# Kernel tuning notes

Hardware: AMD Instinct MI355X
Metric: run time of the kernel (lower is better)

Reference implementation:

```python
import jax, jax.numpy as jnp
import numpy as np

EPS = 1e-08
IN_CH = 256
OUT_CH = 256
STYLE_DIM = 256
B, N = 4, 65536


def setup_inputs() -> dict:
    key = jax.random.key(0)
    k1, k2, k3, k4 = jax.random.split(key, 4)
    x = jax.random.normal(k1, (B, N, IN_CH), dtype=jnp.float32)
    style = jax.random.normal(k2, (B, N, STYLE_DIM), dtype=jnp.float32)
    # base weight: torch.randn(1,1,in,out) * sqrt(2/(1+0.2^2)) / sqrt(in)
    w_scale = np.sqrt(2.0 / (1.0 + 0.2 ** 2)) / np.sqrt(IN_CH)
    weight = jax.random.normal(k3, (IN_CH, OUT_CH), dtype=jnp.float32) * w_scale
    bias = jnp.zeros((OUT_CH,), dtype=jnp.float32)
    # affine Linear(style_dim -> in_channel), kaiming normal fan_in linear: std = 1/sqrt(fan_in)
    affine_w = jax.random.normal(k4, (IN_CH, STYLE_DIM), dtype=jnp.float32) / np.sqrt(STYLE_DIM)
    affine_b = jnp.zeros((IN_CH,), dtype=jnp.float32)
    return {"x": x, "style": style, "weight": weight, "bias": bias,
            "affine_w": affine_w, "affine_b": affine_b}


def reference(x, style, weight, bias, affine_w, affine_b):
    # mod[b,n,i] = affine(style) + 1
    mod = jnp.einsum('bns,is->bni', style, affine_w) + affine_b + 1.0
    # out0[b,n,o] = sum_i x[b,n,i] * mod[b,n,i] * weight[i,o]
    out0 = jnp.einsum('bni,io->bno', x * mod, weight)
    # demod[b,n,o] = rsqrt(sum_i (weight[i,o]*mod[b,n,i])^2 + eps)
    ssq = jnp.einsum('bni,io->bno', mod * mod, weight * weight)  # [B,N,out]
    out = out0 * jax.lax.rsqrt(ssq + EPS)
    return out + bias
```

## Files before the change

### kernel.cpp

```cpp
#include <hip/hip_runtime.h>


#define CH   256
#define BM   64
#define EPS  1e-8f

typedef __attribute__((ext_vector_type(4))) float f32x4;
typedef __attribute__((ext_vector_type(8))) short bf16x8;
typedef __attribute__((ext_vector_type(4))) short s16x4;

__device__ __forceinline__ short f2b(float f) {
    __bf16 h = (__bf16)f;
    return __builtin_bit_cast(short, h);
}
__device__ __forceinline__ float b2f(short b) {
    union { unsigned u; float f; } v;
    v.u = ((unsigned)(unsigned short)b) << 16;
    return v.f;
}
__device__ __forceinline__ int swz(int row, int chunk) {
    return row * 512 + ((chunk ^ (row & 7)) << 4);
}

__global__ void prep_kernel(const float* __restrict__ weight,
                            const float* __restrict__ affw,
                            short* __restrict__ wTb, short* __restrict__ wT2b,
                            short* __restrict__ affwb)
{
    int t = threadIdx.x, b = blockIdx.x;
    float w  = weight[t * CH + b];
    short wb = f2b(w);
    float wf = b2f(wb);
    wTb  [b * CH + t] = wb;
    wT2b [b * CH + t] = f2b(wf * wf);
    affwb[b * CH + t] = f2b(affw[b * CH + t]);
}

__global__ __launch_bounds__(512, 4)
void smod_main(const float* __restrict__ x, const float* __restrict__ style,
               const float* __restrict__ bias, const float* __restrict__ affb,
               const short* __restrict__ wTb, const short* __restrict__ wT2b,
               const short* __restrict__ affwb,
               float* __restrict__ out)
{
    __shared__ __align__(16) unsigned char smem[65536];
    char* regA = (char*)smem;
    char* regB = (char*)smem + 32768;

    const int tid  = threadIdx.x;
    const int lane = tid & 63;
    const int wid  = tid >> 6;
    const int l15  = lane & 15;
    const int lgrp = lane >> 4;
    const int koff = lgrp << 3;
    const long r0  = (long)blockIdx.x * BM;

    const int urow = (wid << 1) + (lane >> 5);
    const int uch  = lane & 31;

    f32x4 sld[4][2];
    #pragma unroll
    for (int k = 0; k < 4; ++k) {
        const float* p = style + (r0 + k * 16 + urow) * CH + uch * 8;
        sld[k][0] = *(const f32x4*)p;
        sld[k][1] = *(const f32x4*)(p + 4);
    }
    f32x4 xld[4][2];
    #pragma unroll
    for (int k = 0; k < 4; ++k) {
        const float* p = x + (r0 + k * 16 + urow) * CH + uch * 8;
        xld[k][0] = *(const f32x4*)p;
        xld[k][1] = *(const f32x4*)(p + 4);
    }
    #pragma unroll
    for (int k = 0; k < 4; ++k) {
        int row = k * 16 + urow;
        bf16x8 v;
        #pragma unroll
        for (int j = 0; j < 8; ++j)
            v[j] = f2b(j < 4 ? sld[k][0][j] : sld[k][1][j - 4]);
        *(bf16x8*)(regA + swz(row, uch)) = v;
    }
    __syncthreads();

    f32x4 accm[2][4];
    #pragma unroll
    for (int a = 0; a < 2; ++a)
        #pragma unroll
        for (int b = 0; b < 4; ++b) { accm[a][b][0]=0.f; accm[a][b][1]=0.f; accm[a][b][2]=0.f; accm[a][b][3]=0.f; }

    #pragma unroll
    for (int kc = 0; kc < 8; ++kc) {
        bf16x8 af[2];
        #pragma unroll
        for (int it = 0; it < 2; ++it)
            af[it] = *(const bf16x8*)(affwb + (wid * 32 + it * 16 + l15) * CH + kc * 32 + koff);
        #pragma unroll
        for (int rt = 0; rt < 4; ++rt) {
            bf16x8 bfr = *(const bf16x8*)(regA + swz(rt * 16 + l15, kc * 4 + lgrp));
            #pragma unroll
            for (int it = 0; it < 2; ++it)
                accm[it][rt] = __builtin_amdgcn_mfma_f32_16x16x32_bf16(
                    af[it], bfr, accm[it][rt], 0, 0, 0);
        }
    }

    #pragma unroll
    for (int it = 0; it < 2; ++it) {
        int i0 = wid * 32 + it * 16 + (lgrp << 2);
        f32x4 ab = *(const f32x4*)(affb + i0);
        int chunk = i0 >> 3;
        int sub   = (i0 & 7) << 1;
        #pragma unroll
        for (int rt = 0; rt < 4; ++rt) {
            int row = rt * 16 + l15;
            f32x4 m = accm[it][rt];
            s16x4 o4 = { f2b(m[0] + ab[0] + 1.0f), f2b(m[1] + ab[1] + 1.0f),
                         f2b(m[2] + ab[2] + 1.0f), f2b(m[3] + ab[3] + 1.0f) };
            *(s16x4*)(regB + swz(row, chunk) + sub) = o4;
        }
    }
    __syncthreads();

    #pragma unroll
    for (int k = 0; k < 4; ++k) {
        int row = k * 16 + urow;
        bf16x8 mb = *(const bf16x8*)(regB + swz(row, uch));
        bf16x8 a1v, a2v;
        #pragma unroll
        for (int j = 0; j < 8; ++j) {
            float mf = b2f(mb[j]);
            float xf = (j < 4) ? xld[k][0][j] : xld[k][1][j - 4];
            a1v[j] = f2b(xf * mf);
            a2v[j] = f2b(mf * mf);
        }
        *(bf16x8*)(regA + swz(row, uch)) = a1v;
        *(bf16x8*)(regB + swz(row, uch)) = a2v;
    }
    __syncthreads();

    f32x4 acc0[4][2], acc1[4][2];
    #pragma unroll
    for (int a = 0; a < 4; ++a)
        #pragma unroll
        for (int b = 0; b < 2; ++b) {
            acc0[a][b][0]=0.f; acc0[a][b][1]=0.f; acc0[a][b][2]=0.f; acc0[a][b][3]=0.f;
            acc1[a][b][0]=0.f; acc1[a][b][1]=0.f; acc1[a][b][2]=0.f; acc1[a][b][3]=0.f;
        }

    #pragma unroll
    for (int kc = 0; kc < 8; ++kc) {
        bf16x8 bw[2], bw2[2];
        #pragma unroll
        for (int ct = 0; ct < 2; ++ct) {
            int o = wid * 32 + ct * 16 + l15;
            bw [ct] = *(const bf16x8*)(wTb  + o * CH + kc * 32 + koff);
            bw2[ct] = *(const bf16x8*)(wT2b + o * CH + kc * 32 + koff);
        }
        #pragma unroll
        for (int rt = 0; rt < 4; ++rt) {
            int row = rt * 16 + l15;
            bf16x8 a1f = *(const bf16x8*)(regA + swz(row, kc * 4 + lgrp));
            bf16x8 a2f = *(const bf16x8*)(regB + swz(row, kc * 4 + lgrp));
            #pragma unroll
            for (int ct = 0; ct < 2; ++ct) {
                acc0[rt][ct] = __builtin_amdgcn_mfma_f32_16x16x32_bf16(
                    a1f, bw[ct],  acc0[rt][ct], 0, 0, 0);
                acc1[rt][ct] = __builtin_amdgcn_mfma_f32_16x16x32_bf16(
                    a2f, bw2[ct], acc1[rt][ct], 0, 0, 0);
            }
        }
    }
    __syncthreads();

    #pragma unroll
    for (int ct = 0; ct < 2; ++ct) {
        int o = wid * 32 + ct * 16 + l15;
        float bs = bias[o];
        int cO = o >> 2, sub = (o & 3) << 2;
        #pragma unroll
        for (int rt = 0; rt < 4; ++rt)
            #pragma unroll
            for (int j = 0; j < 4; ++j) {
                int row = rt * 16 + (lgrp << 2) + j;
                float v = acc0[rt][ct][j] * rsqrtf(acc1[rt][ct][j] + EPS) + bs;
                *(float*)((char*)smem + row * 1024 + (((cO ^ (row & 7)) << 4)) + sub) = v;
            }
    }
    __syncthreads();

    #pragma unroll
    for (int k = 0; k < 8; ++k) {
        int row = (k << 3) + wid;
        f32x4 v = *(const f32x4*)((char*)smem + row * 1024 + ((lane ^ (row & 7)) << 4));
        *(f32x4*)(out + (r0 + row) * CH + (lane << 2)) = v;
    }
}

extern "C" void kernel_launch(void* const* d_in, const int* in_sizes, int n_in,
                              void* d_out, int out_size, void* d_ws, size_t ws_size,
                              hipStream_t stream) {
    const float* x      = (const float*)d_in[0];
    const float* style  = (const float*)d_in[1];
    const float* weight = (const float*)d_in[2];
    const float* bias   = (const float*)d_in[3];
    const float* affw   = (const float*)d_in[4];
    const float* affb   = (const float*)d_in[5];
    float* outp = (float*)d_out;

    short* ws    = (short*)d_ws;
    short* wTb   = ws;
    short* wT2b  = ws + CH * CH;
    short* affwb = ws + 2 * CH * CH;

    prep_kernel<<<dim3(CH), dim3(CH), 0, stream>>>(weight, affw, wTb, wT2b, affwb);

    const int rows = 4 * 65536;
    smod_main<<<dim3(rows / BM), dim3(512), 0, stream>>>(
        x, style, bias, affb, wTb, wT2b, affwb, outp);
}
```

Before: 284.0 us.

## Loop each block over eight row tiles with register prefetch of the next tile

Each block now processes eight consecutive 64-row tiles in a loop instead of one, and launches eight times fewer blocks. While the current tile is being computed, the next tile's style and x values are loaded into registers, so global-load latency overlaps with MFMA work. The second GEMM and its epilogue are split into two 32-row halves. Each half's output staging is placed in LDS regions that the other half's operands do not use, which lowers accumulator register pressure. The costs are more live registers for the prefetched data and a small grid that depends on keeping every CU occupied.

```diff
diff --git a/kernel.cpp b/kernel.cpp
--- a/kernel.cpp
+++ b/kernel.cpp
@@ -3,6 +3,7 @@
 
 #define CH   256
 #define BM   64
+#define NT   8
 #define EPS  1e-8f
 
 typedef __attribute__((ext_vector_type(4))) float f32x4;
@@ -20,6 +21,9 @@
 }
 __device__ __forceinline__ int swz(int row, int chunk) {
     return row * 512 + ((chunk ^ (row & 7)) << 4);
+}
+__device__ __forceinline__ int sbase(int p, int lr) {
+    return p * 16384 + lr * 1024 + ((lr & 16) << 10);
 }
 
 __global__ void prep_kernel(const float* __restrict__ weight,
@@ -53,147 +57,173 @@
     const int l15  = lane & 15;
     const int lgrp = lane >> 4;
     const int koff = lgrp << 3;
-    const long r0  = (long)blockIdx.x * BM;
+    const long rblk = (long)blockIdx.x * (BM * NT);
 
     const int urow = (wid << 1) + (lane >> 5);
     const int uch  = lane & 31;
 
-    f32x4 sld[4][2];
-    #pragma unroll
-    for (int k = 0; k < 4; ++k) {
-        const float* p = style + (r0 + k * 16 + urow) * CH + uch * 8;
-        sld[k][0] = *(const f32x4*)p;
-        sld[k][1] = *(const f32x4*)(p + 4);
+    f32x4 sld[4][2], xld[4][2];
+    {
+        const float* sp = style + rblk * CH;
+        const float* xp = x + rblk * CH;
+        #pragma unroll
+        for (int k = 0; k < 4; ++k) {
+            const float* p = sp + (k * 16 + urow) * CH + uch * 8;
+            sld[k][0] = *(const f32x4*)p;  sld[k][1] = *(const f32x4*)(p + 4);
+        }
+        #pragma unroll
+        for (int k = 0; k < 4; ++k) {
+            const float* p = xp + (k * 16 + urow) * CH + uch * 8;
+            xld[k][0] = *(const f32x4*)p;  xld[k][1] = *(const f32x4*)(p + 4);
+        }
     }
-    f32x4 xld[4][2];
-    #pragma unroll
-    for (int k = 0; k < 4; ++k) {
-        const float* p = x + (r0 + k * 16 + urow) * CH + uch * 8;
-        xld[k][0] = *(const f32x4*)p;
-        xld[k][1] = *(const f32x4*)(p + 4);
-    }
-    #pragma unroll
-    for (int k = 0; k < 4; ++k) {
-        int row = k * 16 + urow;
-        bf16x8 v;
-        #pragma unroll
-        for (int j = 0; j < 8; ++j)
-            v[j] = f2b(j < 4 ? sld[k][0][j] : sld[k][1][j - 4]);
-        *(bf16x8*)(regA + swz(row, uch)) = v;
-    }
-    __syncthreads();
-
-    f32x4 accm[2][4];
-    #pragma unroll
-    for (int a = 0; a < 2; ++a)
-        #pragma unroll
-        for (int b = 0; b < 4; ++b) { accm[a][b][0]=0.f; accm[a][b][1]=0.f; accm[a][b][2]=0.f; accm[a][b][3]=0.f; }
-
-    #pragma unroll
-    for (int kc = 0; kc < 8; ++kc) {
-        bf16x8 af[2];
-        #pragma unroll
-        for (int it = 0; it < 2; ++it)
-            af[it] = *(const bf16x8*)(affwb + (wid * 32 + it * 16 + l15) * CH + kc * 32 + koff);
-        #pragma unroll
-        for (int rt = 0; rt < 4; ++rt) {
-            bf16x8 bfr = *(const bf16x8*)(regA + swz(rt * 16 + l15, kc * 4 + lgrp));
+
+    #pragma unroll 1
+    for (int t = 0; t < NT; ++t) {
+        const long r0 = rblk + (long)t * BM;
+        __syncthreads();
+
+        #pragma unroll
+        for (int k = 0; k < 4; ++k) {
+            int row = k * 16 + urow;
+            bf16x8 v;
+            #pragma unroll
+            for (int j = 0; j < 8; ++j)
+                v[j] = f2b(j < 4 ? sld[k][0][j] : sld[k][1][j - 4]);
+            *(bf16x8*)(regA + swz(row, uch)) = v;
+        }
+        if (t + 1 < NT) {
+            const float* sp = style + (rblk + (long)(t + 1) * BM) * CH;
+            #pragma unroll
+            for (int k = 0; k < 4; ++k) {
+                const float* p = sp + (k * 16 + urow) * CH + uch * 8;
+                sld[k][0] = *(const f32x4*)p;  sld[k][1] = *(const f32x4*)(p + 4);
+            }
+        }
+        __syncthreads();
+
+        f32x4 accm[2][4];
+        #pragma unroll
+        for (int a = 0; a < 2; ++a)
+            #pragma unroll
+            for (int b = 0; b < 4; ++b) { accm[a][b][0]=0.f; accm[a][b][1]=0.f; accm[a][b][2]=0.f; accm[a][b][3]=0.f; }
+
+        #pragma unroll
+        for (int kc = 0; kc < 8; ++kc) {
+            bf16x8 af[2];
             #pragma unroll
             for (int it = 0; it < 2; ++it)
-                accm[it][rt] = __builtin_amdgcn_mfma_f32_16x16x32_bf16(
-                    af[it], bfr, accm[it][rt], 0, 0, 0);
-        }
-    }
-
-    #pragma unroll
-    for (int it = 0; it < 2; ++it) {
-        int i0 = wid * 32 + it * 16 + (lgrp << 2);
-        f32x4 ab = *(const f32x4*)(affb + i0);
-        int chunk = i0 >> 3;
-        int sub   = (i0 & 7) << 1;
-        #pragma unroll
-        for (int rt = 0; rt < 4; ++rt) {
-            int row = rt * 16 + l15;
-            f32x4 m = accm[it][rt];
-            s16x4 o4 = { f2b(m[0] + ab[0] + 1.0f), f2b(m[1] + ab[1] + 1.0f),
-                         f2b(m[2] + ab[2] + 1.0f), f2b(m[3] + ab[3] + 1.0f) };
-            *(s16x4*)(regB + swz(row, chunk) + sub) = o4;
-        }
-    }
-    __syncthreads();
-
-    #pragma unroll
-    for (int k = 0; k < 4; ++k) {
-        int row = k * 16 + urow;
-        bf16x8 mb = *(const bf16x8*)(regB + swz(row, uch));
-        bf16x8 a1v, a2v;
-        #pragma unroll
-        for (int j = 0; j < 8; ++j) {
-            float mf = b2f(mb[j]);
-            float xf = (j < 4) ? xld[k][0][j] : xld[k][1][j - 4];
-            a1v[j] = f2b(xf * mf);
-            a2v[j] = f2b(mf * mf);
-        }
-        *(bf16x8*)(regA + swz(row, uch)) = a1v;
-        *(bf16x8*)(regB + swz(row, uch)) = a2v;
-    }
-    __syncthreads();
-
-    f32x4 acc0[4][2], acc1[4][2];
-    #pragma unroll
-    for (int a = 0; a < 4; ++a)
-        #pragma unroll
-        for (int b = 0; b < 2; ++b) {
-            acc0[a][b][0]=0.f; acc0[a][b][1]=0.f; acc0[a][b][2]=0.f; acc0[a][b][3]=0.f;
-            acc1[a][b][0]=0.f; acc1[a][b][1]=0.f; acc1[a][b][2]=0.f; acc1[a][b][3]=0.f;
-        }
-
-    #pragma unroll
-    for (int kc = 0; kc < 8; ++kc) {
-        bf16x8 bw[2], bw2[2];
-        #pragma unroll
-        for (int ct = 0; ct < 2; ++ct) {
-            int o = wid * 32 + ct * 16 + l15;
-            bw [ct] = *(const bf16x8*)(wTb  + o * CH + kc * 32 + koff);
-            bw2[ct] = *(const bf16x8*)(wT2b + o * CH + kc * 32 + koff);
-        }
-        #pragma unroll
-        for (int rt = 0; rt < 4; ++rt) {
-            int row = rt * 16 + l15;
-            bf16x8 a1f = *(const bf16x8*)(regA + swz(row, kc * 4 + lgrp));
-            bf16x8 a2f = *(const bf16x8*)(regB + swz(row, kc * 4 + lgrp));
+                af[it] = *(const bf16x8*)(affwb + (wid * 32 + it * 16 + l15) * CH + kc * 32 + koff);
+            #pragma unroll
+            for (int rt = 0; rt < 4; ++rt) {
+                bf16x8 bfr = *(const bf16x8*)(regA + swz(rt * 16 + l15, kc * 4 + lgrp));
+                #pragma unroll
+                for (int it = 0; it < 2; ++it)
+                    accm[it][rt] = __builtin_amdgcn_mfma_f32_16x16x32_bf16(
+                        af[it], bfr, accm[it][rt], 0, 0, 0);
+            }
+        }
+        #pragma unroll
+        for (int it = 0; it < 2; ++it) {
+            int i0 = wid * 32 + it * 16 + (lgrp << 2);
+            f32x4 ab = *(const f32x4*)(affb + i0);
+            int chunk = i0 >> 3;
+            int sub   = (i0 & 7) << 1;
+            #pragma unroll
+            for (int rt = 0; rt < 4; ++rt) {
+                int row = rt * 16 + l15;
+                f32x4 m = accm[it][rt];
+                s16x4 o4 = { f2b(m[0] + ab[0] + 1.0f), f2b(m[1] + ab[1] + 1.0f),
+                             f2b(m[2] + ab[2] + 1.0f), f2b(m[3] + ab[3] + 1.0f) };
+                *(s16x4*)(regB + swz(row, chunk) + sub) = o4;
+            }
+        }
+        __syncthreads();
+
+        #pragma unroll
+        for (int k = 0; k < 4; ++k) {
+            int row = k * 16 + urow;
+            bf16x8 mb = *(const bf16x8*)(regB + swz(row, uch));
+            bf16x8 a1v, a2v;
+            #pragma unroll
+            for (int j = 0; j < 8; ++j) {
+                float mf = b2f(mb[j]);
+                float xf = (j < 4) ? xld[k][0][j] : xld[k][1][j - 4];
+                a1v[j] = f2b(xf * mf);
+                a2v[j] = f2b(mf * mf);
+            }
+            *(bf16x8*)(regA + swz(row, uch)) = a1v;
+            *(bf16x8*)(regB + swz(row, uch)) = a2v;
+        }
+        __syncthreads();
+
+        #pragma unroll
+        for (int p = 0; p < 2; ++p) {
+            f32x4 acc0[2][2], acc1[2][2];
+            #pragma unroll
+            for (int a = 0; a < 2; ++a)
+                #pragma unroll
+                for (int b = 0; b < 2; ++b) {
+                    acc0[a][b][0]=0.f; acc0[a][b][1]=0.f; acc0[a][b][2]=0.f; acc0[a][b][3]=0.f;
+                    acc1[a][b][0]=0.f; acc1[a][b][1]=0.f; acc1[a][b][2]=0.f; acc1[a][b][3]=0.f;
+                }
+            #pragma unroll
+            for (int kc = 0; kc < 8; ++kc) {
+                bf16x8 bw[2], bw2[2];
+                #pragma unroll
+                for (int ct = 0; ct < 2; ++ct) {
+                    int o = wid * 32 + ct * 16 + l15;
+                    bw [ct] = *(const bf16x8*)(wTb  + o * CH + kc * 32 + koff);
+                    bw2[ct] = *(const bf16x8*)(wT2b + o * CH + kc * 32 + koff);
+                }
+                #pragma unroll
+                for (int rt = 0; rt < 2; ++rt) {
+                    int row = p * 32 + rt * 16 + l15;
+                    bf16x8 a1f = *(const bf16x8*)(regA + swz(row, kc * 4 + lgrp));
+                    bf16x8 a2f = *(const bf16x8*)(regB + swz(row, kc * 4 + lgrp));
+                    #pragma unroll
+                    for (int ct = 0; ct < 2; ++ct) {
+                        acc0[rt][ct] = __builtin_amdgcn_mfma_f32_16x16x32_bf16(
+                            a1f, bw[ct],  acc0[rt][ct], 0, 0, 0);
+                        acc1[rt][ct] = __builtin_amdgcn_mfma_f32_16x16x32_bf16(
+                            a2f, bw2[ct], acc1[rt][ct], 0, 0, 0);
+                    }
+                }
+            }
+            __syncthreads();
+
+            if (p == 1 && t + 1 < NT) {
+                const float* xp = x + (rblk + (long)(t + 1) * BM) * CH;
+                #pragma unroll
+                for (int k = 0; k < 4; ++k) {
+                    const float* q = xp + (k * 16 + urow) * CH + uch * 8;
+                    xld[k][0] = *(const f32x4*)q;  xld[k][1] = *(const f32x4*)(q + 4);
+                }
+            }
+
             #pragma unroll
             for (int ct = 0; ct < 2; ++ct) {
-                acc0[rt][ct] = __builtin_amdgcn_mfma_f32_16x16x32_bf16(
-                    a1f, bw[ct],  acc0[rt][ct], 0, 0, 0);
-                acc1[rt][ct] = __builtin_amdgcn_mfma_f32_16x16x32_bf16(
-                    a2f, bw2[ct], acc1[rt][ct], 0, 0, 0);
-            }
-        }
-    }
-    __syncthreads();
-
-    #pragma unroll
-    for (int ct = 0; ct < 2; ++ct) {
-        int o = wid * 32 + ct * 16 + l15;
-        float bs = bias[o];
-        int cO = o >> 2, sub = (o & 3) << 2;
-        #pragma unroll
-        for (int rt = 0; rt < 4; ++rt)
-            #pragma unroll
-            for (int j = 0; j < 4; ++j) {
-                int row = rt * 16 + (lgrp << 2) + j;
-                float v = acc0[rt][ct][j] * rsqrtf(acc1[rt][ct][j] + EPS) + bs;
-                *(float*)((char*)smem + row * 1024 + (((cO ^ (row & 7)) << 4)) + sub) = v;
-            }
-    }
-    __syncthreads();
-
-    #pragma unroll
-    for (int k = 0; k < 8; ++k) {
-        int row = (k << 3) + wid;
-        f32x4 v = *(const f32x4*)((char*)smem + row * 1024 + ((lane ^ (row & 7)) << 4));
-        *(f32x4*)(out + (r0 + row) * CH + (lane << 2)) = v;
+                int o = wid * 32 + ct * 16 + l15;
+                float bs = bias[o];
+                int cO = o >> 2, sub = (o & 3) << 2;
+                #pragma unroll
+                for (int rt = 0; rt < 2; ++rt)
+                    #pragma unroll
+                    for (int j = 0; j < 4; ++j) {
+                        int lr = rt * 16 + (lgrp << 2) + j;
+                        float v = acc0[rt][ct][j] * rsqrtf(acc1[rt][ct][j] + EPS) + bs;
+                        *(float*)((char*)smem + sbase(p, lr) + (((cO ^ (lr & 7)) << 4)) + sub) = v;
+                    }
+            }
+            __syncthreads();
+
+            #pragma unroll
+            for (int k = 0; k < 4; ++k) {
+                int lr = (k << 3) + wid;
+                f32x4 v = *(const f32x4*)((char*)smem + sbase(p, lr) + ((lane ^ (lr & 7)) << 4));
+                *(f32x4*)(out + (r0 + p * 32 + lr) * CH + (lane << 2)) = v;
+            }
+        }
     }
 }
 
@@ -216,6 +246,6 @@
     prep_kernel<<<dim3(CH), dim3(CH), 0, stream>>>(weight, affw, wTb, wT2b, affwb);
 
     const int rows = 4 * 65536;
-    smod_main<<<dim3(rows / BM), dim3(512), 0, stream>>>(
+    smod_main<<<dim3(rows / (BM * NT)), dim3(512), 0, stream>>>(
         x, style, bias, affb, wTb, wT2b, affwb, outp);
 }
```

After: 982.6 us. +246.0%, slower.

## Make kernel persistent over row tiles with async LDS prefetch of style

Applied to the files above, without the earlier changes.

The kernel now launches 256 blocks that each loop over 16 tiles of 64 rows, instead of one block per tile. While the current tile is processed, the next tile's style rows are prefetched straight into a dedicated 64KB LDS buffer with global_load_lds DMA. The goal is to overlap the style fetch with the MFMA work and to avoid per-block launch and ramp-up costs. In exchange, LDS per block doubles to 128KB and launch bounds drop, which leaves about one block per CU. The x loads stay synchronous, and the output staging now uses an unswizzled LDS layout that may cause bank conflicts.

```diff
diff --git a/kernel.cpp b/kernel.cpp
--- a/kernel.cpp
+++ b/kernel.cpp
@@ -3,6 +3,7 @@
 
 #define CH   256
 #define BM   64
+#define NT   16
 #define EPS  1e-8f
 
 typedef __attribute__((ext_vector_type(4))) float f32x4;
@@ -20,6 +21,11 @@
 }
 __device__ __forceinline__ int swz(int row, int chunk) {
     return row * 512 + ((chunk ^ (row & 7)) << 4);
+}
+__device__ __forceinline__ void lds_dma16(const float* g, float* l) {
+    __builtin_amdgcn_global_load_lds(
+        (const __attribute__((address_space(1))) unsigned int*)g,
+        (__attribute__((address_space(3))) unsigned int*)l, 16, 0, 0);
 }
 
 __global__ void prep_kernel(const float* __restrict__ weight,
@@ -36,16 +42,18 @@
     affwb[b * CH + t] = f2b(affw[b * CH + t]);
 }
 
-__global__ __launch_bounds__(512, 4)
+__global__ __launch_bounds__(512, 2)
 void smod_main(const float* __restrict__ x, const float* __restrict__ style,
                const float* __restrict__ bias, const float* __restrict__ affb,
                const short* __restrict__ wTb, const short* __restrict__ wT2b,
                const short* __restrict__ affwb,
                float* __restrict__ out)
 {
-    __shared__ __align__(16) unsigned char smem[65536];
-    char* regA = (char*)smem;
-    char* regB = (char*)smem + 32768;
+    __shared__ __align__(16) unsigned char smem[131072];
+    float* sty = (float*)smem;
+    char*  A_s = (char*)smem + 65536;
+    char*  B_s = (char*)smem + 98304;
+    float* st  = (float*)(smem + 65536);
 
     const int tid  = threadIdx.x;
     const int lane = tid & 63;
@@ -53,147 +61,163 @@
     const int l15  = lane & 15;
     const int lgrp = lane >> 4;
     const int koff = lgrp << 3;
-    const long r0  = (long)blockIdx.x * BM;
-
-    const int urow = (wid << 1) + (lane >> 5);
-    const int uch  = lane & 31;
-
-    f32x4 sld[4][2];
-    #pragma unroll
-    for (int k = 0; k < 4; ++k) {
-        const float* p = style + (r0 + k * 16 + urow) * CH + uch * 8;
-        sld[k][0] = *(const f32x4*)p;
-        sld[k][1] = *(const f32x4*)(p + 4);
+    const long rblk = (long)blockIdx.x * (BM * NT);
+
+    {
+        const float* sp = style + rblk * CH;
+        #pragma unroll
+        for (int k = 0; k < 8; ++k) {
+            int seg = wid * 8 + k;
+            lds_dma16(sp + seg * 256 + lane * 4, sty + seg * 256);
+        }
     }
-    f32x4 xld[4][2];
-    #pragma unroll
-    for (int k = 0; k < 4; ++k) {
-        const float* p = x + (r0 + k * 16 + urow) * CH + uch * 8;
-        xld[k][0] = *(const f32x4*)p;
-        xld[k][1] = *(const f32x4*)(p + 4);
-    }
-    #pragma unroll
-    for (int k = 0; k < 4; ++k) {
-        int row = k * 16 + urow;
-        bf16x8 v;
-        #pragma unroll
-        for (int j = 0; j < 8; ++j)
-            v[j] = f2b(j < 4 ? sld[k][0][j] : sld[k][1][j - 4]);
-        *(bf16x8*)(regA + swz(row, uch)) = v;
-    }
-    __syncthreads();
-
-    f32x4 accm[2][4];
-    #pragma unroll
-    for (int a = 0; a < 2; ++a)
-        #pragma unroll
-        for (int b = 0; b < 4; ++b) { accm[a][b][0]=0.f; accm[a][b][1]=0.f; accm[a][b][2]=0.f; accm[a][b][3]=0.f; }
-
-    #pragma unroll
-    for (int kc = 0; kc < 8; ++kc) {
-        bf16x8 af[2];
-        #pragma unroll
-        for (int it = 0; it < 2; ++it)
-            af[it] = *(const bf16x8*)(affwb + (wid * 32 + it * 16 + l15) * CH + kc * 32 + koff);
-        #pragma unroll
-        for (int rt = 0; rt < 4; ++rt) {
-            bf16x8 bfr = *(const bf16x8*)(regA + swz(rt * 16 + l15, kc * 4 + lgrp));
+
+    #pragma unroll 1
+    for (int t = 0; t < NT; ++t) {
+        const long r0 = rblk + (long)t * BM;
+
+        asm volatile("s_waitcnt vmcnt(0)" ::: "memory");
+        __syncthreads();
+
+        f32x4 xld[4][2];
+        #pragma unroll
+        for (int k = 0; k < 4; ++k) {
+            int u = (k << 9) + tid;
+            int row = u >> 5, ch = u & 31;
+            const float* p = x + (r0 + row) * CH + ch * 8;
+            xld[k][0] = *(const f32x4*)p;
+            xld[k][1] = *(const f32x4*)(p + 4);
+        }
+
+        #pragma unroll
+        for (int k = 0; k < 8; ++k) {
+            int u = (k << 9) + tid;
+            int row = u >> 6, c4 = u & 63;
+            f32x4 v = *(const f32x4*)(sty + row * 256 + c4 * 4);
+            s16x4 o = { f2b(v[0]), f2b(v[1]), f2b(v[2]), f2b(v[3]) };
+            *(s16x4*)(A_s + swz(row, c4 >> 1) + ((c4 & 1) << 3)) = o;
+        }
+        __syncthreads();
+
+        if (t + 1 < NT) {
+            const float* sp = style + (rblk + (long)(t + 1) * BM) * CH;
+            #pragma unroll
+            for (int k = 0; k < 8; ++k) {
+                int seg = wid * 8 + k;
+                lds_dma16(sp + seg * 256 + lane * 4, sty + seg * 256);
+            }
+        }
+
+        f32x4 accm[2][4];
+        #pragma unroll
+        for (int a = 0; a < 2; ++a)
+            #pragma unroll
+            for (int b = 0; b < 4; ++b) { accm[a][b][0]=0.f; accm[a][b][1]=0.f; accm[a][b][2]=0.f; accm[a][b][3]=0.f; }
+
+        #pragma unroll
+        for (int kc = 0; kc < 8; ++kc) {
+            bf16x8 af[2];
             #pragma unroll
             for (int it = 0; it < 2; ++it)
-                accm[it][rt] = __builtin_amdgcn_mfma_f32_16x16x32_bf16(
-                    af[it], bfr, accm[it][rt], 0, 0, 0);
-        }
-    }
-
-    #pragma unroll
-    for (int it = 0; it < 2; ++it) {
-        int i0 = wid * 32 + it * 16 + (lgrp << 2);
-        f32x4 ab = *(const f32x4*)(affb + i0);
-        int chunk = i0 >> 3;
-        int sub   = (i0 & 7) << 1;
-        #pragma unroll
-        for (int rt = 0; rt < 4; ++rt) {
-            int row = rt * 16 + l15;
-            f32x4 m = accm[it][rt];
-            s16x4 o4 = { f2b(m[0] + ab[0] + 1.0f), f2b(m[1] + ab[1] + 1.0f),
-                         f2b(m[2] + ab[2] + 1.0f), f2b(m[3] + ab[3] + 1.0f) };
-            *(s16x4*)(regB + swz(row, chunk) + sub) = o4;
-        }
-    }
-    __syncthreads();
-
-    #pragma unroll
-    for (int k = 0; k < 4; ++k) {
-        int row = k * 16 + urow;
-        bf16x8 mb = *(const bf16x8*)(regB + swz(row, uch));
-        bf16x8 a1v, a2v;
-        #pragma unroll
-        for (int j = 0; j < 8; ++j) {
-            float mf = b2f(mb[j]);
-            float xf = (j < 4) ? xld[k][0][j] : xld[k][1][j - 4];
-            a1v[j] = f2b(xf * mf);
-            a2v[j] = f2b(mf * mf);
-        }
-        *(bf16x8*)(regA + swz(row, uch)) = a1v;
-        *(bf16x8*)(regB + swz(row, uch)) = a2v;
-    }
-    __syncthreads();
-
-    f32x4 acc0[4][2], acc1[4][2];
-    #pragma unroll
-    for (int a = 0; a < 4; ++a)
-        #pragma unroll
-        for (int b = 0; b < 2; ++b) {
-            acc0[a][b][0]=0.f; acc0[a][b][1]=0.f; acc0[a][b][2]=0.f; acc0[a][b][3]=0.f;
-            acc1[a][b][0]=0.f; acc1[a][b][1]=0.f; acc1[a][b][2]=0.f; acc1[a][b][3]=0.f;
-        }
-
-    #pragma unroll
-    for (int kc = 0; kc < 8; ++kc) {
-        bf16x8 bw[2], bw2[2];
+                af[it] = *(const bf16x8*)(affwb + (wid * 32 + it * 16 + l15) * CH + kc * 32 + koff);
+            #pragma unroll
+            for (int rt = 0; rt < 4; ++rt) {
+                bf16x8 bfr = *(const bf16x8*)(A_s + swz(rt * 16 + l15, kc * 4 + lgrp));
+                #pragma unroll
+                for (int it = 0; it < 2; ++it)
+                    accm[it][rt] = __builtin_amdgcn_mfma_f32_16x16x32_bf16(
+                        af[it], bfr, accm[it][rt], 0, 0, 0);
+            }
+        }
+        #pragma unroll
+        for (int it = 0; it < 2; ++it) {
+            int i0 = wid * 32 + it * 16 + (lgrp << 2);
+            f32x4 ab = *(const f32x4*)(affb + i0);
+            int chunk = i0 >> 3;
+            int sub   = (i0 & 7) << 1;
+            #pragma unroll
+            for (int rt = 0; rt < 4; ++rt) {
+                int row = rt * 16 + l15;
+                f32x4 m = accm[it][rt];
+                s16x4 o4 = { f2b(m[0] + ab[0] + 1.0f), f2b(m[1] + ab[1] + 1.0f),
+                             f2b(m[2] + ab[2] + 1.0f), f2b(m[3] + ab[3] + 1.0f) };
+                *(s16x4*)(B_s + swz(row, chunk) + sub) = o4;
+            }
+        }
+        __syncthreads();
+
+        #pragma unroll
+        for (int k = 0; k < 4; ++k) {
+            int u = (k << 9) + tid;
+            int row = u >> 5, ch = u & 31;
+            bf16x8 mb = *(const bf16x8*)(B_s + swz(row, ch));
+            bf16x8 a1v, a2v;
+            #pragma unroll
+            for (int j = 0; j < 8; ++j) {
+                float mf = b2f(mb[j]);
+                float xf = (j < 4) ? xld[k][0][j] : xld[k][1][j - 4];
+                a1v[j] = f2b(xf * mf);
+                a2v[j] = f2b(mf * mf);
+            }
+            *(bf16x8*)(A_s + swz(row, ch)) = a1v;
+            *(bf16x8*)(B_s + swz(row, ch)) = a2v;
+        }
+        __syncthreads();
+
+        f32x4 acc0[4][2], acc1[4][2];
+        #pragma unroll
+        for (int a = 0; a < 4; ++a)
+            #pragma unroll
+            for (int b = 0; b < 2; ++b) {
+                acc0[a][b][0]=0.f; acc0[a][b][1]=0.f; acc0[a][b][2]=0.f; acc0[a][b][3]=0.f;
+                acc1[a][b][0]=0.f; acc1[a][b][1]=0.f; acc1[a][b][2]=0.f; acc1[a][b][3]=0.f;
+            }
+
+        #pragma unroll
+        for (int kc = 0; kc < 8; ++kc) {
+            bf16x8 bw[2], bw2[2];
+            #pragma unroll
+            for (int ct = 0; ct < 2; ++ct) {
+                int o = wid * 32 + ct * 16 + l15;
+                bw [ct] = *(const bf16x8*)(wTb  + o * CH + kc * 32 + koff);
+                bw2[ct] = *(const bf16x8*)(wT2b + o * CH + kc * 32 + koff);
+            }
+            #pragma unroll
+            for (int rt = 0; rt < 4; ++rt) {
+                bf16x8 a1f = *(const bf16x8*)(A_s + swz(rt * 16 + l15, kc * 4 + lgrp));
+                bf16x8 a2f = *(const bf16x8*)(B_s + swz(rt * 16 + l15, kc * 4 + lgrp));
+                #pragma unroll
+                for (int ct = 0; ct < 2; ++ct) {
+                    acc0[rt][ct] = __builtin_amdgcn_mfma_f32_16x16x32_bf16(
+                        a1f, bw[ct],  acc0[rt][ct], 0, 0, 0);
+                    acc1[rt][ct] = __builtin_amdgcn_mfma_f32_16x16x32_bf16(
+                        a2f, bw2[ct], acc1[rt][ct], 0, 0, 0);
+                }
+            }
+        }
+        __syncthreads();
+
         #pragma unroll
         for (int ct = 0; ct < 2; ++ct) {
             int o = wid * 32 + ct * 16 + l15;
-            bw [ct] = *(const bf16x8*)(wTb  + o * CH + kc * 32 + koff);
-            bw2[ct] = *(const bf16x8*)(wT2b + o * CH + kc * 32 + koff);
-        }
-        #pragma unroll
-        for (int rt = 0; rt < 4; ++rt) {
-            int row = rt * 16 + l15;
-            bf16x8 a1f = *(const bf16x8*)(regA + swz(row, kc * 4 + lgrp));
-            bf16x8 a2f = *(const bf16x8*)(regB + swz(row, kc * 4 + lgrp));
-            #pragma unroll
-            for (int ct = 0; ct < 2; ++ct) {
-                acc0[rt][ct] = __builtin_amdgcn_mfma_f32_16x16x32_bf16(
-                    a1f, bw[ct],  acc0[rt][ct], 0, 0, 0);
-                acc1[rt][ct] = __builtin_amdgcn_mfma_f32_16x16x32_bf16(
-                    a2f, bw2[ct], acc1[rt][ct], 0, 0, 0);
-            }
-        }
-    }
-    __syncthreads();
-
-    #pragma unroll
-    for (int ct = 0; ct < 2; ++ct) {
-        int o = wid * 32 + ct * 16 + l15;
-        float bs = bias[o];
-        int cO = o >> 2, sub = (o & 3) << 2;
-        #pragma unroll
-        for (int rt = 0; rt < 4; ++rt)
-            #pragma unroll
-            for (int j = 0; j < 4; ++j) {
-                int row = rt * 16 + (lgrp << 2) + j;
-                float v = acc0[rt][ct][j] * rsqrtf(acc1[rt][ct][j] + EPS) + bs;
-                *(float*)((char*)smem + row * 1024 + (((cO ^ (row & 7)) << 4)) + sub) = v;
-            }
-    }
-    __syncthreads();
-
-    #pragma unroll
-    for (int k = 0; k < 8; ++k) {
-        int row = (k << 3) + wid;
-        f32x4 v = *(const f32x4*)((char*)smem + row * 1024 + ((lane ^ (row & 7)) << 4));
-        *(f32x4*)(out + (r0 + row) * CH + (lane << 2)) = v;
+            float bsv = bias[o];
+            #pragma unroll
+            for (int rt = 0; rt < 4; ++rt)
+                #pragma unroll
+                for (int j = 0; j < 4; ++j) {
+                    int row = rt * 16 + (lgrp << 2) + j;
+                    st[row * 256 + o] = acc0[rt][ct][j] * rsqrtf(acc1[rt][ct][j] + EPS) + bsv;
+                }
+        }
+        __syncthreads();
+
+        #pragma unroll
+        for (int k = 0; k < 8; ++k) {
+            int u = (k << 9) + tid;
+            int row = u >> 6, c4 = u & 63;
+            f32x4 v = *(const f32x4*)(st + row * 256 + c4 * 4);
+            *(f32x4*)(out + (r0 + row) * CH + c4 * 4) = v;
+        }
     }
 }
 
@@ -215,7 +239,6 @@
 
     prep_kernel<<<dim3(CH), dim3(CH), 0, stream>>>(weight, affw, wTb, wT2b, affwb);
 
-    const int rows = 4 * 65536;
-    smod_main<<<dim3(rows / BM), dim3(512), 0, stream>>>(
+    smod_main<<<dim3(256), dim3(512), 0, stream>>>(
         x, style, bias, affb, wTb, wT2b, affwb, outp);
 }
```

Result: slower. 353.3 us (+24.4%).
